# Kernel tuning notes

Hardware: AMD Instinct MI355X
Metric: run time of the kernel (lower is better)

Reference implementation:

```python
import jax, jax.numpy as jnp
import numpy as np

NEG_INF = -1000000000.0

N, T, D, H = 2, 4096, 512, 8
S = D // H  # size_per_head = 64


def setup_inputs() -> dict:
    key = jax.random.key(0)
    ks = jax.random.split(key, 6)
    scale = 1.0 / np.sqrt(D)
    return {
        "query": jax.random.normal(ks[0], (N, T, D), dtype=jnp.float32),
        "reference": jax.random.normal(ks[1], (N, T, D), dtype=jnp.float32),
        "padding_mask": jnp.zeros((N, 1, 1, T), dtype=jnp.float32),
        "Wq": jax.random.normal(ks[2], (D, H, S), dtype=jnp.float32) * scale,
        "Wk": jax.random.normal(ks[3], (D, H, S), dtype=jnp.float32) * scale,
        "Wv": jax.random.normal(ks[4], (D, H, S), dtype=jnp.float32) * scale,
        "Wo": jax.random.normal(ks[5], (H, S, D), dtype=jnp.float32) * scale,
    }


def reference(query, reference, padding_mask, Wq, Wk, Wv, Wo):
    # split projections: [N,T,D] x [D,H,S] -> [N,T,H,S]
    q = jnp.einsum("NTD,DHS->NTHS", query, Wq) * (S ** -0.5)
    k = jnp.einsum("NTD,DHS->NTHS", reference, Wk)
    v = jnp.einsum("NTD,DHS->NTHS", reference, Wv)
    # scores [N,H,Q,R]; mask is 0/1, scaled by NEG_INF (as in source)
    scores = jnp.einsum("NQHS,NRHS->NHQR", q, k) + padding_mask * NEG_INF
    probs = jax.nn.softmax(scores, axis=3)
    # dropout is identity (training=False)
    ctx = jnp.einsum("NHQR,NRHS->NQHS", probs, v)
    # merge projection: [N,Q,H,S] x [H,S,D] -> [N,Q,D]
    return jnp.einsum("NTHS,HSD->NTD", ctx, Wo)
```

## Files before the change

kernel.cpp:

```cpp
#include <hip/hip_runtime.h>
#include <stdint.h>

using u16    = unsigned short;
using u32    = unsigned int;
using short8 = __attribute__((ext_vector_type(8))) short;
using s16x4  = __attribute__((ext_vector_type(4))) short;
using f32x4  = __attribute__((ext_vector_type(4))) float;
using f32x16 = __attribute__((ext_vector_type(16))) float;
using i32x4  = __attribute__((ext_vector_type(4))) int;

constexpr float LOG2E = 1.44269504088896340736f;


__device__ __forceinline__ u16 f2bf(float f) {
  uint32_t u = __builtin_bit_cast(uint32_t, f);
  return (u16)((u + 0x7fffu + ((u >> 16) & 1u)) >> 16);
}

__device__ __forceinline__ void gload16(const void* g, void* l) {
  __builtin_amdgcn_global_load_lds(
      (const __attribute__((address_space(1))) unsigned int*)g,
      (__attribute__((address_space(3))) unsigned int*)l, 16, 0, 0);
}

__device__ __forceinline__ u32 cvtpk_bf16(float lo, float hi) {
  u32 r;
  asm("v_cvt_pk_bf16_f32 %0, %1, %2" : "=v"(r) : "v"(lo), "v"(hi));
  return r;
}

__device__ __forceinline__ f32x16 zero16() {
  f32x16 z;
#pragma unroll
  for (int i = 0; i < 16; ++i) z[i] = 0.f;
  return z;
}

__device__ __forceinline__ short8 ldfrag(const u16* s, int row, int kbyte) {
  int phys = (row << 7) + (kbyte ^ ((row & 7) << 4));
  return *(const short8*)((const char*)s + phys);
}

__global__ __launch_bounds__(256) void prep_kernel(
    const float4* __restrict__ qin, const float4* __restrict__ rin,
    const float* __restrict__ mask,
    const float* __restrict__ wq, const float* __restrict__ wk,
    const float* __restrict__ wv, const float* __restrict__ wo,
    u16* __restrict__ xq, u16* __restrict__ xr,
    u16* __restrict__ wqt, u16* __restrict__ wkt,
    u16* __restrict__ wvt, u16* __restrict__ wot,
    u16* __restrict__ kfr, int* __restrict__ mflag) {
  const int gid = blockIdx.x * blockDim.x + threadIdx.x;
  const int stride = gridDim.x * blockDim.x;
  for (int i = gid; i < (2 * 4096 * 512) / 4; i += stride) {
    float4 a = qin[i], b = rin[i];
    s16x4 va = {(short)f2bf(a.x), (short)f2bf(a.y), (short)f2bf(a.z), (short)f2bf(a.w)};
    s16x4 vb = {(short)f2bf(b.x), (short)f2bf(b.y), (short)f2bf(b.z), (short)f2bf(b.w)};
    *(s16x4*)(xq + i * 4) = va;
    *(s16x4*)(xr + i * 4) = vb;
  }
  for (int i = gid; i < 512 * 512; i += stride) {
    int orow = i >> 9, ocol = i & 511;
    int si = ocol * 512 + orow;
    wqt[i] = f2bf(wq[si]);
    wkt[i] = f2bf(wk[si]);
    wvt[i] = f2bf(wv[si]);
    wot[i] = f2bf(wo[si]);
  }
  for (int i = gid; i < 16 * 4096; i += stride) {
    int head = i >> 12, key = i & 4095;
    int nn = head >> 3;
    float mv = mask[nn * 4096 + key];
    float mt = mv * (-1.0e9f * LOG2E);
    int tile = key >> 5, lqk = key & 31;
    u16* base = kfr + (((size_t)(head * 128 + tile)) * 5 + 4) * 512;
    u16* p0 = base + (size_t)lqk * 8;
    u16* p1 = base + (size_t)(32 + lqk) * 8;
    p0[0] = f2bf(mt);
#pragma unroll
    for (int j = 1; j < 8; ++j) p0[j] = 0;
#pragma unroll
    for (int j = 0; j < 8; ++j) p1[j] = 0;
    unsigned long long any = __ballot(mv != 0.0f);
    if ((threadIdx.x & 63) == 0 && any != 0ULL) atomicOr(mflag, 1);
  }
}

__device__ __forceinline__ void gemm_core(const u16* __restrict__ A, const u16* __restrict__ Bt,
                                          int K, u16* As, u16* Bs, int tm0, int tn0,
                                          f32x4 acc[4][4]) {
  const int tid = threadIdx.x;
  const int wv = tid >> 6, ln = tid & 63;
  const int lr = ln & 15, hi = ln >> 4;
  const int wr = wv >> 1, wc = wv & 1;
  const size_t rowbytes = (size_t)K * 2;
  for (int k0 = 0; k0 < K; k0 += 64) {
    __syncthreads();
    const char* Ab = (const char*)A + (size_t)tm0 * rowbytes + (size_t)k0 * 2;
    const char* Bb = (const char*)Bt + (size_t)tn0 * rowbytes + (size_t)k0 * 2;
#pragma unroll
    for (int c = 0; c < 4; ++c) {
      int lin = wv * 4096 + c * 1024 + ln * 16;
      int row = lin >> 7;
      int cb = (lin & 127) ^ ((row & 7) << 4);
      gload16(Ab + (size_t)row * rowbytes + cb, (char*)As + wv * 4096 + c * 1024);
      gload16(Bb + (size_t)row * rowbytes + cb, (char*)Bs + wv * 4096 + c * 1024);
    }
    __syncthreads();
#pragma unroll
    for (int ks = 0; ks < 2; ++ks) {
      short8 af[4], bf[4];
#pragma unroll
      for (int m = 0; m < 4; ++m) af[m] = ldfrag(As, wr * 64 + m * 16 + lr, ks * 64 + hi * 16);
#pragma unroll
      for (int n = 0; n < 4; ++n) bf[n] = ldfrag(Bs, wc * 64 + n * 16 + lr, ks * 64 + hi * 16);
#pragma unroll
      for (int m = 0; m < 4; ++m)
#pragma unroll
        for (int n = 0; n < 4; ++n)
          acc[m][n] = __builtin_amdgcn_mfma_f32_16x16x32_bf16(af[m], bf[n], acc[m][n], 0, 0, 0);
    }
  }
}

__global__ __launch_bounds__(256) void qkv_gemm(
    const u16* __restrict__ xq, const u16* __restrict__ xr,
    const u16* __restrict__ wqt, const u16* __restrict__ wkt, const u16* __restrict__ wvt,
    u16* __restrict__ qo, u16* __restrict__ kfr, u16* __restrict__ vfr) {
  __shared__ u16 As[128 * 64];
  __shared__ u16 Bs[128 * 64];
  const int z = blockIdx.z;
  const u16* A  = (z == 0) ? xq : xr;
  const u16* Bt = (z == 0) ? wqt : (z == 1) ? wkt : wvt;
  const int tm0 = blockIdx.x * 128, tn0 = blockIdx.y * 128;
  f32x4 acc[4][4];
#pragma unroll
  for (int m = 0; m < 4; ++m)
#pragma unroll
    for (int n = 0; n < 4; ++n) { f32x4 zz = {0.f, 0.f, 0.f, 0.f}; acc[m][n] = zz; }
  gemm_core(A, Bt, 512, As, Bs, tm0, tn0, acc);

  const int tid = threadIdx.x, wv = tid >> 6, ln = tid & 63, lr = ln & 15, hi = ln >> 4;
  const int wr = wv >> 1, wc = wv & 1;
  const float scale = (z == 0) ? 0.125f * LOG2E : 1.0f;
#pragma unroll
  for (int m = 0; m < 4; ++m) {
#pragma unroll
    for (int n = 0; n < 4; ++n) {
#pragma unroll
      for (int r = 0; r < 4; ++r) {
        int rg = tm0 + wr * 64 + m * 16 + hi * 4 + r;
        int cg = tn0 + wc * 64 + n * 16 + lr;
        int nb = rg >> 12, t = rg & 4095;
        int h = cg >> 6, s = cg & 63;
        int head = nb * 8 + h;
        u16 b = f2bf(acc[m][n][r] * scale);
        if (z == 0) {
          qo[((size_t)head * 4096 + t) * 64 + s] = b;
        } else if (z == 1) {
          int tile = t >> 5, lqk = t & 31;
          int ks = s >> 4, hh = (s >> 3) & 1, j = s & 7;
          kfr[((((size_t)(head * 128 + tile)) * 5 + ks) * 64 + hh * 32 + lqk) * 8 + j] = b;
        } else {
          int tile = t >> 5, w5 = t & 31;
          int ks = w5 >> 4, hh = (w5 >> 3) & 1, j = w5 & 7;
          int st = s >> 5, lqs = s & 31;
          vfr[((((size_t)(head * 128 + tile)) * 4 + ks * 2 + st) * 64 + hh * 32 + lqs) * 8 + j] = b;
        }
      }
    }
  }
}

__global__ __launch_bounds__(512, 2) void attn12_kernel(
    const u16* __restrict__ q, const char* __restrict__ kfr, const char* __restrict__ vfr,
    u16* __restrict__ ctx, const int* __restrict__ mflag) {
  __shared__ float cmb[4][32][64];
  __shared__ float cl[4][64];
  const int id = blockIdx.x;
  const int xcd = id & 7, slot = id >> 3;
  const int head = xcd * 2 + (slot >> 4);
  const int qb = slot & 15;
  const int n = head >> 3, h = head & 7;
  const int tid = threadIdx.x, wv = tid >> 6, ln = tid & 63;
  const int lq = ln & 31, hi = ln >> 5, hi4 = hi * 4;
  const int qt = wv & 3, kg = wv >> 2;
  const int q0 = qb * 256 + qt * 64;
  const bool aug = (*mflag != 0);

  short8 qfa[5], qfb[5];
  {
    const char* qp = (const char*)(q + (size_t)head * 4096 * 64) + (size_t)(q0 + lq) * 128 + hi * 16;
#pragma unroll
    for (int ks = 0; ks < 4; ++ks) {
      qfa[ks] = *(const short8*)(qp + ks * 32);
      qfb[ks] = *(const short8*)(qp + 32 * 128 + ks * 32);
    }
    short8 z = {0, 0, 0, 0, 0, 0, 0, 0};
    if (hi == 0) z[0] = (short)0x3F80;
    qfa[4] = z;
    qfb[4] = z;
  }

  const char* kp = kfr + (size_t)head * 655360 + (size_t)(kg * 64) * 5120 + ln * 16;
  const char* vp = vfr + (size_t)head * 524288 + (size_t)(kg * 64) * 4096 + ln * 16;

  short8 kA[5];
#pragma unroll
  for (int s = 0; s < 4; ++s) kA[s] = *(const short8*)(kp + s * 1024);
  if (aug) kA[4] = *(const short8*)(kp + 4 * 1024);
  kp += 5120;

  f32x16 cacc0a = zero16(), cacc1a = zero16();
  f32x16 cacc0b = zero16(), cacc1b = zero16();
  float lra = 0.f, lrb = 0.f;

  for (int it = 0; it < 64; ++it) {
    short8 vA[4];
#pragma unroll
    for (int s = 0; s < 4; ++s) vA[s] = *(const short8*)(vp + s * 1024);
    vp += 4096;

    f32x16 Sa = zero16(), Sb = zero16();
    __builtin_amdgcn_s_setprio(1);
#pragma unroll
    for (int ks = 0; ks < 4; ++ks) {
      Sa = __builtin_amdgcn_mfma_f32_32x32x16_bf16(kA[ks], qfa[ks], Sa, 0, 0, 0);
      Sb = __builtin_amdgcn_mfma_f32_32x32x16_bf16(kA[ks], qfb[ks], Sb, 0, 0, 0);
    }
    if (aug) {
      Sa = __builtin_amdgcn_mfma_f32_32x32x16_bf16(kA[4], qfa[4], Sa, 0, 0, 0);
      Sb = __builtin_amdgcn_mfma_f32_32x32x16_bf16(kA[4], qfb[4], Sb, 0, 0, 0);
    }
    __builtin_amdgcn_s_setprio(0);

    short8 kN[5];
#pragma unroll
    for (int s = 0; s < 4; ++s) kN[s] = *(const short8*)(kp + s * 1024);
    if (aug) kN[4] = *(const short8*)(kp + 4 * 1024);
    kp += 5120;

    float pa_[16], pb_[16];
#pragma unroll
    for (int r = 0; r < 16; ++r) pa_[r] = __builtin_amdgcn_exp2f(Sa[r]);
#pragma unroll
    for (int r = 0; r < 16; ++r) pb_[r] = __builtin_amdgcn_exp2f(Sb[r]);
    {
      float ta[16], tb[16];
#pragma unroll
      for (int r = 0; r < 16; ++r) { ta[r] = pa_[r]; tb[r] = pb_[r]; }
#pragma unroll
      for (int d = 8; d > 0; d >>= 1)
#pragma unroll
        for (int r = 0; r < d; ++r) { ta[r] += ta[r + d]; tb[r] += tb[r + d]; }
      lra += ta[0] + __shfl_xor(ta[0], 32);
      lrb += tb[0] + __shfl_xor(tb[0], 32);
    }

    short8 pa0, pa1, pb0, pb1;
#define SHF32(x) ((u32)__shfl_xor((int)(x), 32))
#define MKFRAGS(P, FA, FB)                                                          \
    {                                                                               \
      u32 A01 = cvtpk_bf16(P[0], P[1]), B23 = cvtpk_bf16(P[2], P[3]);               \
      u32 C45 = cvtpk_bf16(P[4], P[5]), D67 = cvtpk_bf16(P[6], P[7]);               \
      u32 E89 = cvtpk_bf16(P[8], P[9]), F01 = cvtpk_bf16(P[10], P[11]);             \
      u32 G23 = cvtpk_bf16(P[12], P[13]), H45 = cvtpk_bf16(P[14], P[15]);           \
      u32 A01x = SHF32(A01), B23x = SHF32(B23), C45x = SHF32(C45), D67x = SHF32(D67);\
      u32 E89x = SHF32(E89), F01x = SHF32(F01), G23x = SHF32(G23), H45x = SHF32(H45);\
      i32x4 fa = {(int)(hi ? C45x : A01), (int)(hi ? D67x : B23),                   \
                  (int)(hi ? C45 : A01x), (int)(hi ? D67 : B23x)};                  \
      i32x4 fb = {(int)(hi ? G23x : E89), (int)(hi ? H45x : F01),                   \
                  (int)(hi ? G23 : E89x), (int)(hi ? H45 : F01x)};                  \
      FA = __builtin_bit_cast(short8, fa);                                          \
      FB = __builtin_bit_cast(short8, fb);                                          \
    }
    MKFRAGS(pa_, pa0, pa1);
    MKFRAGS(pb_, pb0, pb1);
#undef MKFRAGS
#undef SHF32

    __builtin_amdgcn_s_setprio(1);
    cacc0a = __builtin_amdgcn_mfma_f32_32x32x16_bf16(pa0, vA[0], cacc0a, 0, 0, 0);
    cacc1a = __builtin_amdgcn_mfma_f32_32x32x16_bf16(pa0, vA[1], cacc1a, 0, 0, 0);
    cacc0b = __builtin_amdgcn_mfma_f32_32x32x16_bf16(pb0, vA[0], cacc0b, 0, 0, 0);
    cacc1b = __builtin_amdgcn_mfma_f32_32x32x16_bf16(pb0, vA[1], cacc1b, 0, 0, 0);
    cacc0a = __builtin_amdgcn_mfma_f32_32x32x16_bf16(pa1, vA[2], cacc0a, 0, 0, 0);
    cacc1a = __builtin_amdgcn_mfma_f32_32x32x16_bf16(pa1, vA[3], cacc1a, 0, 0, 0);
    cacc0b = __builtin_amdgcn_mfma_f32_32x32x16_bf16(pb1, vA[2], cacc0b, 0, 0, 0);
    cacc1b = __builtin_amdgcn_mfma_f32_32x32x16_bf16(pb1, vA[3], cacc1b, 0, 0, 0);
    __builtin_amdgcn_s_setprio(0);

#pragma unroll
    for (int s = 0; s < 4; ++s) kA[s] = kN[s];
    if (aug) kA[4] = kN[4];
  }

  u16* cp = ctx + (size_t)(n * 4096 + q0) * 512 + h * 64;
  if (kg == 1) {
#pragma unroll
    for (int r = 0; r < 16; ++r) {
      cmb[qt][r][ln] = cacc0a[r];
      cmb[qt][r + 16][ln] = cacc1a[r];
    }
    cl[qt][ln] = lra;
  }
  __syncthreads();
  if (kg == 0) {
#pragma unroll
    for (int r = 0; r < 16; ++r) {
      cacc0a[r] += cmb[qt][r][ln];
      cacc1a[r] += cmb[qt][r + 16][ln];
    }
    lra += cl[qt][ln];
    float li = 1.0f / lra;
    int lii = __builtin_bit_cast(int, li);
#pragma unroll
    for (int r = 0; r < 16; ++r) {
      int cr = (r & 3) + ((r >> 2) << 3) + hi4;
      float inv = __builtin_bit_cast(float, __builtin_amdgcn_ds_bpermute(cr << 2, lii));
      cp[(size_t)cr * 512 + lq] = f2bf(cacc0a[r] * inv);
      cp[(size_t)cr * 512 + 32 + lq] = f2bf(cacc1a[r] * inv);
    }
  }
  __syncthreads();
  if (kg == 1) {
#pragma unroll
    for (int r = 0; r < 16; ++r) {
      cmb[qt][r][ln] = cacc0b[r];
      cmb[qt][r + 16][ln] = cacc1b[r];
    }
    cl[qt][ln] = lrb;
  }
  __syncthreads();
  if (kg == 0) {
#pragma unroll
    for (int r = 0; r < 16; ++r) {
      cacc0b[r] += cmb[qt][r][ln];
      cacc1b[r] += cmb[qt][r + 16][ln];
    }
    lrb += cl[qt][ln];
    float li = 1.0f / lrb;
    int lii = __builtin_bit_cast(int, li);
    u16* cpb = cp + (size_t)32 * 512;
#pragma unroll
    for (int r = 0; r < 16; ++r) {
      int cr = (r & 3) + ((r >> 2) << 3) + hi4;
      float inv = __builtin_bit_cast(float, __builtin_amdgcn_ds_bpermute(cr << 2, lii));
      cpb[(size_t)cr * 512 + lq] = f2bf(cacc0b[r] * inv);
      cpb[(size_t)cr * 512 + 32 + lq] = f2bf(cacc1b[r] * inv);
    }
  }
}

__global__ __launch_bounds__(256) void out_gemm(
    const u16* __restrict__ ctx, const u16* __restrict__ wot, float* __restrict__ out) {
  __shared__ u16 As[128 * 64];
  __shared__ u16 Bs[128 * 64];
  const int tm0 = blockIdx.x * 128, tn0 = blockIdx.y * 128;
  f32x4 acc[4][4];
#pragma unroll
  for (int m = 0; m < 4; ++m)
#pragma unroll
    for (int n = 0; n < 4; ++n) { f32x4 zz = {0.f, 0.f, 0.f, 0.f}; acc[m][n] = zz; }
  gemm_core(ctx, wot, 512, As, Bs, tm0, tn0, acc);

  const int tid = threadIdx.x, wv = tid >> 6, ln = tid & 63, lr = ln & 15, hi = ln >> 4;
  const int wr = wv >> 1, wc = wv & 1;
#pragma unroll
  for (int m = 0; m < 4; ++m)
#pragma unroll
    for (int n = 0; n < 4; ++n)
#pragma unroll
      for (int r = 0; r < 4; ++r) {
        int rg = tm0 + wr * 64 + m * 16 + hi * 4 + r;
        int cg = tn0 + wc * 64 + n * 16 + lr;
        out[(size_t)rg * 512 + cg] = acc[m][n][r];
      }
}

extern "C" void kernel_launch(void* const* d_in, const int* in_sizes, int n_in,
                              void* d_out, int out_size, void* d_ws, size_t ws_size,
                              hipStream_t stream) {
  (void)in_sizes; (void)n_in; (void)out_size; (void)ws_size;
  const float* qin  = (const float*)d_in[0];
  const float* rin  = (const float*)d_in[1];
  const float* mask = (const float*)d_in[2];
  const float* wq   = (const float*)d_in[3];
  const float* wk   = (const float*)d_in[4];
  const float* wv   = (const float*)d_in[5];
  const float* wo   = (const float*)d_in[6];

  char* ws = (char*)d_ws;
  u16* xq   = (u16*)(ws + 0);
  u16* ctx  = (u16*)(ws + 0);
  u16* xr   = (u16*)(ws + 8388608);
  u16* wqt  = (u16*)(ws + 16777216);
  u16* wkt  = (u16*)(ws + 17301504);
  u16* wvt  = (u16*)(ws + 17825792);
  u16* wot  = (u16*)(ws + 18350080);
  u16* qo   = (u16*)(ws + 18874368);
  u16* kfr  = (u16*)(ws + 27262976);
  u16* vfr  = (u16*)(ws + 37748736);
  int* mflag = (int*)(ws + 46137344);

  hipMemsetAsync(mflag, 0, 4, stream);
  prep_kernel<<<2048, 256, 0, stream>>>((const float4*)qin, (const float4*)rin, mask,
                                        wq, wk, wv, wo, xq, xr, wqt, wkt, wvt, wot,
                                        kfr, mflag);
  qkv_gemm<<<dim3(64, 4, 3), 256, 0, stream>>>(xq, xr, wqt, wkt, wvt, qo, kfr, vfr);
  attn12_kernel<<<256, 512, 0, stream>>>(qo, (const char*)kfr, (const char*)vfr, ctx, mflag);
  out_gemm<<<dim3(64, 4), 256, 0, stream>>>(ctx, wot, (float*)d_out);
}
```

Baseline: 138.9 us.

## Split attention KV range across four wave groups and double block count

The attention kernel now gives each block 128 queries instead of 256. Its 8 waves form 2 query tiles by 4 key groups, and each key group covers a quarter of the keys, so the kernel launches 512 blocks instead of 256. Partial context accumulators and row sums from three key groups are combined through larger shared memory into group 0. This is meant to fill the 256 CUs more evenly and shorten the serial loop per wave. In exchange, every Q fragment is loaded by twice as many blocks, and the cross-wave reduction costs more shared memory and sync work.

```diff
diff --git a/kernel.cpp b/kernel.cpp
--- a/kernel.cpp
+++ b/kernel.cpp
@@ -172,20 +172,20 @@
   }
 }
 
-__global__ __launch_bounds__(512, 2) void attn12_kernel(
+__global__ __launch_bounds__(512, 2) void attn13_kernel(
     const u16* __restrict__ q, const char* __restrict__ kfr, const char* __restrict__ vfr,
     u16* __restrict__ ctx, const int* __restrict__ mflag) {
-  __shared__ float cmb[4][32][64];
-  __shared__ float cl[4][64];
+  __shared__ float cmb[2][3][32][64];
+  __shared__ float cl[2][3][64];
   const int id = blockIdx.x;
   const int xcd = id & 7, slot = id >> 3;
-  const int head = xcd * 2 + (slot >> 4);
-  const int qb = slot & 15;
+  const int head = xcd * 2 + (slot >> 5);
+  const int qb = slot & 31;
   const int n = head >> 3, h = head & 7;
   const int tid = threadIdx.x, wv = tid >> 6, ln = tid & 63;
   const int lq = ln & 31, hi = ln >> 5, hi4 = hi * 4;
-  const int qt = wv & 3, kg = wv >> 2;
-  const int q0 = qb * 256 + qt * 64;
+  const int qt = wv & 1, kg = wv >> 1;
+  const int q0 = qb * 128 + qt * 64;
   const bool aug = (*mflag != 0);
 
   short8 qfa[5], qfb[5];
@@ -202,8 +202,8 @@
     qfb[4] = z;
   }
 
-  const char* kp = kfr + (size_t)head * 655360 + (size_t)(kg * 64) * 5120 + ln * 16;
-  const char* vp = vfr + (size_t)head * 524288 + (size_t)(kg * 64) * 4096 + ln * 16;
+  const char* kp = kfr + (size_t)head * 655360 + (size_t)(kg * 32) * 5120 + ln * 16;
+  const char* vp = vfr + (size_t)head * 524288 + (size_t)(kg * 32) * 4096 + ln * 16;
 
   short8 kA[5];
 #pragma unroll
@@ -215,7 +215,7 @@
   f32x16 cacc0b = zero16(), cacc1b = zero16();
   float lra = 0.f, lrb = 0.f;
 
-  for (int it = 0; it < 64; ++it) {
+  for (int it = 0; it < 32; ++it) {
     short8 vA[4];
 #pragma unroll
     for (int s = 0; s < 4; ++s) vA[s] = *(const short8*)(vp + s * 1024);
@@ -296,22 +296,25 @@
   }
 
   u16* cp = ctx + (size_t)(n * 4096 + q0) * 512 + h * 64;
-  if (kg == 1) {
+  if (kg != 0) {
 #pragma unroll
     for (int r = 0; r < 16; ++r) {
-      cmb[qt][r][ln] = cacc0a[r];
-      cmb[qt][r + 16][ln] = cacc1a[r];
-    }
-    cl[qt][ln] = lra;
+      cmb[qt][kg - 1][r][ln] = cacc0a[r];
+      cmb[qt][kg - 1][r + 16][ln] = cacc1a[r];
+    }
+    cl[qt][kg - 1][ln] = lra;
   }
   __syncthreads();
   if (kg == 0) {
 #pragma unroll
-    for (int r = 0; r < 16; ++r) {
-      cacc0a[r] += cmb[qt][r][ln];
-      cacc1a[r] += cmb[qt][r + 16][ln];
-    }
-    lra += cl[qt][ln];
+    for (int g = 0; g < 3; ++g) {
+#pragma unroll
+      for (int r = 0; r < 16; ++r) {
+        cacc0a[r] += cmb[qt][g][r][ln];
+        cacc1a[r] += cmb[qt][g][r + 16][ln];
+      }
+      lra += cl[qt][g][ln];
+    }
     float li = 1.0f / lra;
     int lii = __builtin_bit_cast(int, li);
 #pragma unroll
@@ -323,22 +326,25 @@
     }
   }
   __syncthreads();
-  if (kg == 1) {
+  if (kg != 0) {
 #pragma unroll
     for (int r = 0; r < 16; ++r) {
-      cmb[qt][r][ln] = cacc0b[r];
-      cmb[qt][r + 16][ln] = cacc1b[r];
-    }
-    cl[qt][ln] = lrb;
+      cmb[qt][kg - 1][r][ln] = cacc0b[r];
+      cmb[qt][kg - 1][r + 16][ln] = cacc1b[r];
+    }
+    cl[qt][kg - 1][ln] = lrb;
   }
   __syncthreads();
   if (kg == 0) {
 #pragma unroll
-    for (int r = 0; r < 16; ++r) {
-      cacc0b[r] += cmb[qt][r][ln];
-      cacc1b[r] += cmb[qt][r + 16][ln];
-    }
-    lrb += cl[qt][ln];
+    for (int g = 0; g < 3; ++g) {
+#pragma unroll
+      for (int r = 0; r < 16; ++r) {
+        cacc0b[r] += cmb[qt][g][r][ln];
+        cacc1b[r] += cmb[qt][g][r + 16][ln];
+      }
+      lrb += cl[qt][g][ln];
+    }
     float li = 1.0f / lrb;
     int lii = __builtin_bit_cast(int, li);
     u16* cpb = cp + (size_t)32 * 512;
@@ -408,6 +414,6 @@
                                         wq, wk, wv, wo, xq, xr, wqt, wkt, wvt, wot,
                                         kfr, mflag);
   qkv_gemm<<<dim3(64, 4, 3), 256, 0, stream>>>(xq, xr, wqt, wkt, wvt, qo, kfr, vfr);
-  attn12_kernel<<<256, 512, 0, stream>>>(qo, (const char*)kfr, (const char*)vfr, ctx, mflag);
+  attn13_kernel<<<512, 512, 0, stream>>>(qo, (const char*)kfr, (const char*)vfr, ctx, mflag);
   out_gemm<<<dim3(64, 4), 256, 0, stream>>>(ctx, wot, (float*)d_out);
 }
```

Result: slower. 144.8 us (+4.2%).
